# Performance work log

Hardware: AMD Instinct MI355X
Metric: run time of the kernel (lower is better)

Reference implementation:

```python
import jax, jax.numpy as jnp
import numpy as np

# Fixed-point precision used by the MPC framework (fractional bits).
FRAC_BITS = 16
SCALE = float(2 ** FRAC_BITS)

def quantize(v):
    """Snap a real value to the fixed-point grid with f fractional bits
    (models SharedPair fixedpoint / dup_with_precision truncation)."""
    return jnp.round(v * SCALE) / SCALE

def setup_inputs() -> dict:
    key = jax.random.key(0)
    k1, k2 = jax.random.split(key)
    B, D_in, D_out = 8192, 1024, 1024
    x = jax.random.normal(k1, (B, D_in), dtype=jnp.float32)
    # weight init: normal(scale=1/sqrt(D_in+1)) as in the module
    w = jax.random.normal(k2, (D_in, D_out), dtype=jnp.float32) * np.float32(1.0 / np.sqrt(D_in + 1))
    b = jnp.zeros((D_out,), dtype=jnp.float32)
    # inputs/params live on the fixed-point grid in the MPC protocol
    return {"x": quantize(x), "w": quantize(w), "b": b}

def reference(x, w, b):
    # BilinearTriangle.compute_u(x, w) with f_xy = a @ b is a Beaver-triple
    # secure matmul; its plaintext semantics is exactly x @ w (result at
    # doubled fixed-point precision 2f).
    y = x @ w + b  # b is dup_with_precision'ed to y.fixedpoint; same value
    # drelu_binary(y): secure comparison producing the sign bit s = (y > 0)
    s = (y > 0).astype(y.dtype)
    out = y * s  # relu(y, s)
    # dup_with_precision(x[0].fixedpoint): truncate back to f fractional bits
    return quantize(out)
```

## Files before the change

kernel.cpp:

```cpp
#include <hip/hip_runtime.h>
#include <hip/hip_bf16.h>
#include <stdint.h>


typedef __attribute__((ext_vector_type(8))) short short8;
typedef __attribute__((ext_vector_type(4))) float f32x4;
typedef __attribute__((ext_vector_type(8))) unsigned short us8;

template <int N> struct IC { static constexpr int v = N; };

__device__ __forceinline__ unsigned short f32_to_bf16_rne(float f) {
    uint32_t u = __float_as_uint(f);
    uint32_t r = u + 0x7FFFu + ((u >> 16) & 1u);
    return (unsigned short)(r >> 16);
}
__device__ __forceinline__ float bf16_to_f32(unsigned short s) {
    return __uint_as_float(((uint32_t)s) << 16);
}

__global__ __launch_bounds__(256) void split_x_kernel(const float* __restrict__ x,
                                                      unsigned short* __restrict__ A2) {
    int i = blockIdx.x * 256 + threadIdx.x;
    int e = i * 8;
    int row = e >> 10;
    int col = e & 1023;
    float4 v0 = reinterpret_cast<const float4*>(x)[2 * i];
    float4 v1 = reinterpret_cast<const float4*>(x)[2 * i + 1];
    float vv[8] = {v0.x, v0.y, v0.z, v0.w, v1.x, v1.y, v1.z, v1.w};
    us8 h, m;
    unsigned short* hp = (unsigned short*)&h;
    unsigned short* mp = (unsigned short*)&m;
#pragma unroll
    for (int j = 0; j < 8; ++j) {
        float f = vv[j];
        unsigned short hb = f32_to_bf16_rne(f);
        float r1 = f - bf16_to_f32(hb);
        unsigned short mb = f32_to_bf16_rne(r1);
        hp[j] = hb; mp[j] = mb;
    }
    size_t base = (size_t)row * 2048 + col;
    *reinterpret_cast<us8*>(&A2[base])        = h;
    *reinterpret_cast<us8*>(&A2[base + 1024]) = m;
}

__global__ __launch_bounds__(1024) void split_w_kernel(const float* __restrict__ w,
                                                       unsigned short* __restrict__ Bt2) {
    __shared__ float ts[32][33];
    int tx = threadIdx.x, ty = threadIdx.y;
    int n0 = blockIdx.x * 32, k0 = blockIdx.y * 32;
    ts[ty][tx] = w[(size_t)(k0 + ty) * 1024 + (n0 + tx)];
    __syncthreads();
    float f = ts[tx][ty];
    unsigned short h = f32_to_bf16_rne(f);
    float r = f - bf16_to_f32(h);
    unsigned short l = f32_to_bf16_rne(r);
    int n = n0 + ty, k = k0 + tx;
    Bt2[(size_t)n * 2048 + k]        = h;
    Bt2[(size_t)n * 2048 + 1024 + k] = l;
}

#define BM 256
#define BN 128
#define BK 64
#define NT 48

__device__ __forceinline__ void load16_to_lds(const void* g, void* l) {
    __builtin_amdgcn_global_load_lds(
        (const __attribute__((address_space(1))) unsigned int*)g,
        (__attribute__((address_space(3))) unsigned int*)l,
        16, 0, 0);
}

__device__ __forceinline__ void rd4(short8* dst, const void* base, const int* offs) {
#pragma unroll
    for (int f = 0; f < 4; ++f)
        dst[f] = *reinterpret_cast<const short8*>((const char*)base + offs[f]);
}

__device__ __forceinline__ void mfma16(f32x4 (&acc)[4][4], const short8* af, const short8* bf) {
#pragma unroll
    for (int i = 0; i < 4; ++i)
#pragma unroll
        for (int j = 0; j < 4; ++j)
            acc[i][j] = __builtin_amdgcn_mfma_f32_16x16x32_bf16(af[i], bf[j], acc[i][j], 0, 0, 0);
}

__global__ __launch_bounds__(512, 2) void gemm_kernel(const unsigned short* __restrict__ A2,
                                                      const unsigned short* __restrict__ Bt2,
                                                      const float* __restrict__ bias,
                                                      float* __restrict__ out) {
    __shared__ unsigned short As[3][BM * BK];
    __shared__ unsigned short Bs[3][BN * BK];

    const int tid  = threadIdx.x;
    const int lane = tid & 63;
    const int wave = tid >> 6;
    const int wr = wave >> 1, wc = wave & 1;

    const int bid = blockIdx.x;
    const int wg  = (bid & 7) * 32 + (bid >> 3);
    const int bm = wg >> 3, bn = wg & 7;
    const int m0 = bm * BM, n0 = bn * BN;

    f32x4 acc[4][4];
#pragma unroll
    for (int i = 0; i < 4; ++i)
#pragma unroll
        for (int j = 0; j < 4; ++j) acc[i][j] = (f32x4)0.0f;

    int a0[4], a1[4], b0[4], b1[4];
    {
        const int ch0 = lane >> 4, ch1 = 4 + (lane >> 4);
#pragma unroll
        for (int f = 0; f < 4; ++f) {
            int ar = wr * 64 + f * 16 + (lane & 15);
            a0[f] = ar * 128 + ((ch0 ^ (ar & 7)) << 4);
            a1[f] = ar * 128 + ((ch1 ^ (ar & 7)) << 4);
            int br = wc * 64 + f * 16 + (lane & 15);
            b0[f] = br * 128 + ((ch0 ^ (br & 7)) << 4);
            b1[f] = br * 128 + ((ch1 ^ (br & 7)) << 4);
        }
    }
    int aTh[4], bTh[2];
#pragma unroll
    for (int it = 0; it < 4; ++it) {
        int c = it * 512 + tid, row = c >> 3, sw = (c & 7) ^ (row & 7);
        aTh[it] = (m0 + row) * 2048 + sw * 8;
    }
#pragma unroll
    for (int it = 0; it < 2; ++it) {
        int c = it * 512 + tid, row = c >> 3, sw = (c & 7) ^ (row & 7);
        bTh[it] = (n0 + row) * 2048 + sw * 8;
    }
    const int dst16 = tid * 16;

    auto aoff_of = [](int t) { int blk = t >> 4; return ((blk == 1) ? 1024 : 0) + (t & 15) * 64; };
    auto boff_of = [](int t) { int blk = t >> 4; return ((blk == 2) ? 1024 : 0) + (t & 15) * 64; };

    auto tile = [&](auto BC, auto NBC, int t, bool doStage) {
        constexpr int B  = decltype(BC)::v;
        constexpr int NB = decltype(NBC)::v;
        short8 af[4], bf[4];
        rd4(af, As[B], a0);
        rd4(bf, Bs[B], b0);
        if (doStage) {
            const unsigned short* pA_ = A2 + aoff_of(t + 2);
            load16_to_lds(pA_ + aTh[0], (char*)As[NB] + 0 * 8192 + dst16);
            load16_to_lds(pA_ + aTh[1], (char*)As[NB] + 1 * 8192 + dst16);
            load16_to_lds(pA_ + aTh[2], (char*)As[NB] + 2 * 8192 + dst16);
        }
        __builtin_amdgcn_s_barrier();
        __builtin_amdgcn_s_setprio(1);
        mfma16(acc, af, bf);
        __builtin_amdgcn_s_setprio(0);
        __builtin_amdgcn_s_barrier();
        rd4(af, As[B], a1);
        rd4(bf, Bs[B], b1);
        if (doStage) {
            const unsigned short* pA_ = A2 + aoff_of(t + 2);
            const unsigned short* pB_ = Bt2 + boff_of(t + 2);
            load16_to_lds(pA_ + aTh[3], (char*)As[NB] + 3 * 8192 + dst16);
            load16_to_lds(pB_ + bTh[0], (char*)Bs[NB] + 0 * 8192 + dst16);
            load16_to_lds(pB_ + bTh[1], (char*)Bs[NB] + 1 * 8192 + dst16);
        }
        __builtin_amdgcn_s_barrier();
        __builtin_amdgcn_s_setprio(1);
        mfma16(acc, af, bf);
        __builtin_amdgcn_s_setprio(0);
        asm volatile("s_waitcnt lgkmcnt(0)" ::: "memory");
    };

    {
        const unsigned short* pA_ = A2 + aoff_of(0);
        const unsigned short* pB_ = Bt2 + boff_of(0);
        load16_to_lds(pA_ + aTh[0], (char*)As[0] + 0 * 8192 + dst16);
        load16_to_lds(pA_ + aTh[1], (char*)As[0] + 1 * 8192 + dst16);
        load16_to_lds(pA_ + aTh[2], (char*)As[0] + 2 * 8192 + dst16);
        load16_to_lds(pA_ + aTh[3], (char*)As[0] + 3 * 8192 + dst16);
        load16_to_lds(pB_ + bTh[0], (char*)Bs[0] + 0 * 8192 + dst16);
        load16_to_lds(pB_ + bTh[1], (char*)Bs[0] + 1 * 8192 + dst16);
        const unsigned short* qA_ = A2 + aoff_of(1);
        const unsigned short* qB_ = Bt2 + boff_of(1);
        load16_to_lds(qA_ + aTh[0], (char*)As[1] + 0 * 8192 + dst16);
        load16_to_lds(qA_ + aTh[1], (char*)As[1] + 1 * 8192 + dst16);
        load16_to_lds(qA_ + aTh[2], (char*)As[1] + 2 * 8192 + dst16);
        load16_to_lds(qA_ + aTh[3], (char*)As[1] + 3 * 8192 + dst16);
        load16_to_lds(qB_ + bTh[0], (char*)Bs[1] + 0 * 8192 + dst16);
        load16_to_lds(qB_ + bTh[1], (char*)Bs[1] + 1 * 8192 + dst16);
    }
    asm volatile("s_waitcnt vmcnt(6)" ::: "memory");
    __builtin_amdgcn_s_barrier();

#pragma unroll 1
    for (int tt = 0; tt < 15; ++tt) {
        const int t = tt * 3;
        tile(IC<0>{}, IC<2>{}, t, true);
        asm volatile("s_waitcnt vmcnt(6)" ::: "memory");
        __builtin_amdgcn_s_barrier();
        tile(IC<1>{}, IC<0>{}, t + 1, true);
        asm volatile("s_waitcnt vmcnt(6)" ::: "memory");
        __builtin_amdgcn_s_barrier();
        tile(IC<2>{}, IC<1>{}, t + 2, true);
        asm volatile("s_waitcnt vmcnt(6)" ::: "memory");
        __builtin_amdgcn_s_barrier();
    }
    tile(IC<0>{}, IC<2>{}, 45, true);
    asm volatile("s_waitcnt vmcnt(6)" ::: "memory");
    __builtin_amdgcn_s_barrier();
    tile(IC<1>{}, IC<0>{}, 46, false);
    asm volatile("s_waitcnt vmcnt(0)" ::: "memory");
    __builtin_amdgcn_s_barrier();
    tile(IC<2>{}, IC<0>{}, 47, false);

    const int colBase = n0 + wc * 64 + (lane & 15);
    const int rowBase = m0 + wr * 64 + ((lane >> 4) << 2);
#pragma unroll
    for (int i = 0; i < 4; ++i) {
#pragma unroll
        for (int j = 0; j < 4; ++j) {
            int col = colBase + j * 16;
            float bv = bias[col];
#pragma unroll
            for (int r = 0; r < 4; ++r) {
                int row = rowBase + i * 16 + r;
                float y = acc[i][j][r] + bv;
                y = fmaxf(y, 0.0f);
                y = rintf(y * 65536.0f) * (1.0f / 65536.0f);
                out[(size_t)row * 1024 + col] = y;
            }
        }
    }
}

__global__ __launch_bounds__(256) void naive_kernel(const float* __restrict__ x,
                                                    const float* __restrict__ w,
                                                    const float* __restrict__ bias,
                                                    float* __restrict__ out) {
    int idx = blockIdx.x * 256 + threadIdx.x;
    int row = idx >> 10, col = idx & 1023;
    float s = bias[col];
    for (int k = 0; k < 1024; ++k)
        s += x[(size_t)row * 1024 + k] * w[(size_t)k * 1024 + col];
    s = fmaxf(s, 0.0f);
    out[idx] = rintf(s * 65536.0f) * (1.0f / 65536.0f);
}

extern "C" void kernel_launch(void* const* d_in, const int* in_sizes, int n_in,
                              void* d_out, int out_size, void* d_ws, size_t ws_size,
                              hipStream_t stream) {
    const float* x = (const float*)d_in[0];
    const float* w = (const float*)d_in[1];
    const float* b = (const float*)d_in[2];
    float* out = (float*)d_out;

    const size_t needA = (size_t)8192 * 2048 * 2;
    const size_t needB = (size_t)1024 * 2048 * 2;
    if (ws_size < needA + needB) {
        naive_kernel<<<(8192 * 1024) / 256, 256, 0, stream>>>(x, w, b, out);
        return;
    }
    unsigned short* A2  = (unsigned short*)d_ws;
    unsigned short* Bt2 = (unsigned short*)((char*)d_ws + needA);

    split_x_kernel<<<(8192 * 1024 / 8) / 256, 256, 0, stream>>>(x, A2);
    split_w_kernel<<<dim3(32, 32), dim3(32, 32), 0, stream>>>(w, Bt2);
    gemm_kernel<<<256, 512, 0, stream>>>(A2, Bt2, b, out);
}
```

Before: 150.1 us.

## Load B fragments directly from global into registers, drop B LDS staging

Removes the shared-memory buffers for the B operand. Each wave now loads its B fragments straight from global memory into double-buffered registers one tile ahead, while A keeps its triple-buffered LDS pipeline. The per-tile schedule is also restructured from two half-K MFMA phases with four barriers into one phase with a single barrier. This cuts LDS traffic, LDS capacity and barriers, at the cost of more VGPRs and redundant global loads of B across the four waves that share each column, which may hurt occupancy or latency hiding.

After: 206.9 us. 1.38x slower.

```diff
diff --git a/kernel.cpp b/kernel.cpp
--- a/kernel.cpp
+++ b/kernel.cpp
@@ -77,20 +77,11 @@
         dst[f] = *reinterpret_cast<const short8*>((const char*)base + offs[f]);
 }
 
-__device__ __forceinline__ void mfma16(f32x4 (&acc)[4][4], const short8* af, const short8* bf) {
-#pragma unroll
-    for (int i = 0; i < 4; ++i)
-#pragma unroll
-        for (int j = 0; j < 4; ++j)
-            acc[i][j] = __builtin_amdgcn_mfma_f32_16x16x32_bf16(af[i], bf[j], acc[i][j], 0, 0, 0);
-}
-
 __global__ __launch_bounds__(512, 2) void gemm_kernel(const unsigned short* __restrict__ A2,
                                                       const unsigned short* __restrict__ Bt2,
                                                       const float* __restrict__ bias,
                                                       float* __restrict__ out) {
     __shared__ unsigned short As[3][BM * BK];
-    __shared__ unsigned short Bs[3][BN * BK];
 
     const int tid  = threadIdx.x;
     const int lane = tid & 63;
@@ -108,7 +99,7 @@
 #pragma unroll
         for (int j = 0; j < 4; ++j) acc[i][j] = (f32x4)0.0f;
 
-    int a0[4], a1[4], b0[4], b1[4];
+    int a0[4], a1[4];
     {
         const int ch0 = lane >> 4, ch1 = 4 + (lane >> 4);
 #pragma unroll
@@ -116,101 +107,106 @@
             int ar = wr * 64 + f * 16 + (lane & 15);
             a0[f] = ar * 128 + ((ch0 ^ (ar & 7)) << 4);
             a1[f] = ar * 128 + ((ch1 ^ (ar & 7)) << 4);
-            int br = wc * 64 + f * 16 + (lane & 15);
-            b0[f] = br * 128 + ((ch0 ^ (br & 7)) << 4);
-            b1[f] = br * 128 + ((ch1 ^ (br & 7)) << 4);
-        }
-    }
-    int aTh[4], bTh[2];
+        }
+    }
+    int aTh[4];
 #pragma unroll
     for (int it = 0; it < 4; ++it) {
         int c = it * 512 + tid, row = c >> 3, sw = (c & 7) ^ (row & 7);
         aTh[it] = (m0 + row) * 2048 + sw * 8;
     }
-#pragma unroll
-    for (int it = 0; it < 2; ++it) {
-        int c = it * 512 + tid, row = c >> 3, sw = (c & 7) ^ (row & 7);
-        bTh[it] = (n0 + row) * 2048 + sw * 8;
-    }
     const int dst16 = tid * 16;
+
+    int bOff[8];
+#pragma unroll
+    for (int f = 0; f < 8; ++f) {
+        int brow = n0 + wc * 64 + (f & 3) * 16 + (lane & 15);
+        int ch   = (f >> 2) * 4 + (lane >> 4);
+        bOff[f]  = brow * 2048 + ch * 8;
+    }
 
     auto aoff_of = [](int t) { int blk = t >> 4; return ((blk == 1) ? 1024 : 0) + (t & 15) * 64; };
     auto boff_of = [](int t) { int blk = t >> 4; return ((blk == 2) ? 1024 : 0) + (t & 15) * 64; };
 
-    auto tile = [&](auto BC, auto NBC, int t, bool doStage) {
-        constexpr int B  = decltype(BC)::v;
-        constexpr int NB = decltype(NBC)::v;
-        short8 af[4], bf[4];
-        rd4(af, As[B], a0);
-        rd4(bf, Bs[B], b0);
-        if (doStage) {
+    short8 bA[8], bB[8];
+
+    auto tile = [&](auto LBC, auto RBC, int t, bool doA, bool doB) {
+        constexpr int LB = decltype(LBC)::v;
+        constexpr int NB = (LB + 2) % 3;
+        constexpr int RB = decltype(RBC)::v;
+        short8 (&bc)[8] = *(RB == 0 ? &bA : &bB);
+        short8 (&bl)[8] = *(RB == 0 ? &bB : &bA);
+        short8 af0[4], af1[4];
+        rd4(af0, As[LB], a0);
+        rd4(af1, As[LB], a1);
+        if (doB) {
+            const unsigned short* bp = Bt2 + boff_of(t + 1);
+#pragma unroll
+            for (int f = 0; f < 8; ++f)
+                bl[f] = *reinterpret_cast<const short8*>(bp + bOff[f]);
+        }
+        if (doA) {
             const unsigned short* pA_ = A2 + aoff_of(t + 2);
-            load16_to_lds(pA_ + aTh[0], (char*)As[NB] + 0 * 8192 + dst16);
-            load16_to_lds(pA_ + aTh[1], (char*)As[NB] + 1 * 8192 + dst16);
-            load16_to_lds(pA_ + aTh[2], (char*)As[NB] + 2 * 8192 + dst16);
-        }
-        __builtin_amdgcn_s_barrier();
+#pragma unroll
+            for (int it = 0; it < 4; ++it)
+                load16_to_lds(pA_ + aTh[it], (char*)As[NB] + it * 8192 + dst16);
+        }
         __builtin_amdgcn_s_setprio(1);
-        mfma16(acc, af, bf);
+#pragma unroll
+        for (int i = 0; i < 4; ++i)
+#pragma unroll
+            for (int j = 0; j < 4; ++j)
+                acc[i][j] = __builtin_amdgcn_mfma_f32_16x16x32_bf16(af0[i], bc[j], acc[i][j], 0, 0, 0);
+#pragma unroll
+        for (int i = 0; i < 4; ++i)
+#pragma unroll
+            for (int j = 0; j < 4; ++j)
+                acc[i][j] = __builtin_amdgcn_mfma_f32_16x16x32_bf16(af1[i], bc[4 + j], acc[i][j], 0, 0, 0);
         __builtin_amdgcn_s_setprio(0);
-        __builtin_amdgcn_s_barrier();
-        rd4(af, As[B], a1);
-        rd4(bf, Bs[B], b1);
-        if (doStage) {
-            const unsigned short* pA_ = A2 + aoff_of(t + 2);
-            const unsigned short* pB_ = Bt2 + boff_of(t + 2);
-            load16_to_lds(pA_ + aTh[3], (char*)As[NB] + 3 * 8192 + dst16);
-            load16_to_lds(pB_ + bTh[0], (char*)Bs[NB] + 0 * 8192 + dst16);
-            load16_to_lds(pB_ + bTh[1], (char*)Bs[NB] + 1 * 8192 + dst16);
-        }
-        __builtin_amdgcn_s_barrier();
-        __builtin_amdgcn_s_setprio(1);
-        mfma16(acc, af, bf);
-        __builtin_amdgcn_s_setprio(0);
-        asm volatile("s_waitcnt lgkmcnt(0)" ::: "memory");
+        if (doA) {
+            asm volatile("s_waitcnt vmcnt(4)" ::: "memory");
+        } else if (doB) {
+            asm volatile("s_waitcnt vmcnt(0)" ::: "memory");
+        }
+        if (doA || doB) {
+            asm volatile("s_waitcnt lgkmcnt(0)" ::: "memory");
+            __builtin_amdgcn_s_barrier();
+        }
     };
 
     {
         const unsigned short* pA_ = A2 + aoff_of(0);
-        const unsigned short* pB_ = Bt2 + boff_of(0);
-        load16_to_lds(pA_ + aTh[0], (char*)As[0] + 0 * 8192 + dst16);
-        load16_to_lds(pA_ + aTh[1], (char*)As[0] + 1 * 8192 + dst16);
-        load16_to_lds(pA_ + aTh[2], (char*)As[0] + 2 * 8192 + dst16);
-        load16_to_lds(pA_ + aTh[3], (char*)As[0] + 3 * 8192 + dst16);
-        load16_to_lds(pB_ + bTh[0], (char*)Bs[0] + 0 * 8192 + dst16);
-        load16_to_lds(pB_ + bTh[1], (char*)Bs[0] + 1 * 8192 + dst16);
+#pragma unroll
+        for (int it = 0; it < 4; ++it)
+            load16_to_lds(pA_ + aTh[it], (char*)As[0] + it * 8192 + dst16);
+        const unsigned short* bp = Bt2 + boff_of(0);
+#pragma unroll
+        for (int f = 0; f < 8; ++f)
+            bA[f] = *reinterpret_cast<const short8*>(bp + bOff[f]);
         const unsigned short* qA_ = A2 + aoff_of(1);
-        const unsigned short* qB_ = Bt2 + boff_of(1);
-        load16_to_lds(qA_ + aTh[0], (char*)As[1] + 0 * 8192 + dst16);
-        load16_to_lds(qA_ + aTh[1], (char*)As[1] + 1 * 8192 + dst16);
-        load16_to_lds(qA_ + aTh[2], (char*)As[1] + 2 * 8192 + dst16);
-        load16_to_lds(qA_ + aTh[3], (char*)As[1] + 3 * 8192 + dst16);
-        load16_to_lds(qB_ + bTh[0], (char*)Bs[1] + 0 * 8192 + dst16);
-        load16_to_lds(qB_ + bTh[1], (char*)Bs[1] + 1 * 8192 + dst16);
-    }
-    asm volatile("s_waitcnt vmcnt(6)" ::: "memory");
+#pragma unroll
+        for (int it = 0; it < 4; ++it)
+            load16_to_lds(qA_ + aTh[it], (char*)As[1] + it * 8192 + dst16);
+    }
+    asm volatile("s_waitcnt vmcnt(4)" ::: "memory");
     __builtin_amdgcn_s_barrier();
 
 #pragma unroll 1
-    for (int tt = 0; tt < 15; ++tt) {
-        const int t = tt * 3;
-        tile(IC<0>{}, IC<2>{}, t, true);
-        asm volatile("s_waitcnt vmcnt(6)" ::: "memory");
-        __builtin_amdgcn_s_barrier();
-        tile(IC<1>{}, IC<0>{}, t + 1, true);
-        asm volatile("s_waitcnt vmcnt(6)" ::: "memory");
-        __builtin_amdgcn_s_barrier();
-        tile(IC<2>{}, IC<1>{}, t + 2, true);
-        asm volatile("s_waitcnt vmcnt(6)" ::: "memory");
-        __builtin_amdgcn_s_barrier();
-    }
-    tile(IC<0>{}, IC<2>{}, 45, true);
-    asm volatile("s_waitcnt vmcnt(6)" ::: "memory");
-    __builtin_amdgcn_s_barrier();
-    tile(IC<1>{}, IC<0>{}, 46, false);
-    asm volatile("s_waitcnt vmcnt(0)" ::: "memory");
-    __builtin_amdgcn_s_barrier();
-    tile(IC<2>{}, IC<0>{}, 47, false);
+    for (int tt = 0; tt < 7; ++tt) {
+        const int t = tt * 6;
+        tile(IC<0>{}, IC<0>{}, t + 0, true, true);
+        tile(IC<1>{}, IC<1>{}, t + 1, true, true);
+        tile(IC<2>{}, IC<0>{}, t + 2, true, true);
+        tile(IC<0>{}, IC<1>{}, t + 3, true, true);
+        tile(IC<1>{}, IC<0>{}, t + 4, true, true);
+        tile(IC<2>{}, IC<1>{}, t + 5, true, true);
+    }
+    tile(IC<0>{}, IC<0>{}, 42, true, true);
+    tile(IC<1>{}, IC<1>{}, 43, true, true);
+    tile(IC<2>{}, IC<0>{}, 44, true, true);
+    tile(IC<0>{}, IC<1>{}, 45, true, true);
+    tile(IC<1>{}, IC<0>{}, 46, false, true);
+    tile(IC<2>{}, IC<1>{}, 47, false, false);
 
     const int colBase = n0 + wc * 64 + (lane & 15);
     const int rowBase = m0 + wr * 64 + ((lane >> 4) << 2);
```
